# Performance work log

Measured on AMD Instinct MI355X. Metric: run time of the kernel, lower is better.

Reference implementation:

```python
import jax, jax.numpy as jnp
import numpy as np

N, F, H, Z = 80, 64, 256, 128
OFF = N * (N - 1) // 2  # 3160
E = 800
MPM_ITERS = 50


def _gcn(x, src, dst, W, b, n):
    # PyG GCNConv: add self-loops, symmetric normalization D^-1/2 (A+I) D^-1/2, then +bias
    h = x @ W
    ones = jnp.ones(src.shape[0], dtype=h.dtype)
    deg = jax.ops.segment_sum(ones, dst, num_segments=n)
    dinv = jax.lax.rsqrt(jnp.maximum(deg, 1e-12))
    norm = dinv[src] * dinv[dst]
    out = jax.ops.segment_sum(h[src] * norm[:, None], dst, num_segments=n)
    return out + b


def _bn(h, g, b):
    # BatchNorm1d, training mode (biased batch stats), eps=1e-5
    m = h.mean(0)
    v = ((h - m) ** 2).mean(0)
    return g * (h - m) * jax.lax.rsqrt(v + 1e-5) + b


def setup_inputs() -> dict:
    key = jax.random.key(0)
    ks = jax.random.split(key, 32)
    rn = lambda k, s, sc=0.05: (jax.random.normal(k, s, dtype=jnp.float32) * sc)
    inp = {
        'x': jax.random.normal(ks[0], (N, F), dtype=jnp.float32),
        'edge_index': jax.random.randint(ks[1], (2, E), 0, N, dtype=jnp.int32),
        'adj': jax.random.randint(ks[2], (N, N), 0, 2, dtype=jnp.int32),
        'eps': jax.random.normal(ks[3], (1, Z), dtype=jnp.float32),
        'W1': rn(ks[4], (F, H)), 'b1': jnp.zeros((H,), jnp.float32),
        'g1': jnp.ones((H,), jnp.float32), 'bt1': jnp.zeros((H,), jnp.float32),
        'W2': rn(ks[5], (H, H)), 'b2': jnp.zeros((H,), jnp.float32),
        'g2': jnp.ones((H,), jnp.float32), 'bt2': jnp.zeros((H,), jnp.float32),
        'Wmu': rn(ks[6], (H, Z)), 'bmu': jnp.zeros((Z,), jnp.float32),
        'Wlv': rn(ks[7], (H, Z)), 'blv': jnp.zeros((Z,), jnp.float32),
        'We1': rn(ks[8], (Z, H)), 'be1': jnp.zeros((H,), jnp.float32),
        'We2': rn(ks[9], (H, OFF)), 'be2': jnp.zeros((OFF,), jnp.float32),
        'Wn1': rn(ks[10], (Z, H)), 'bn1': jnp.zeros((H,), jnp.float32),
        'Wn2': rn(ks[11], (H, N)), 'bn2': jnp.zeros((N,), jnp.float32),
    }
    return inp


def reference(x, edge_index, adj, eps, W1, b1, g1, bt1, W2, b2, g2, bt2,
              Wmu, bmu, Wlv, blv, We1, be1, We2, be2, Wn1, bn1, Wn2, bn2):
    n = N
    # ---- encoder: GCN -> BN -> ReLU (x2), mean pool over real nodes ----
    sl = jnp.arange(n, dtype=edge_index.dtype)
    src = jnp.concatenate([edge_index[0], sl])
    dst = jnp.concatenate([edge_index[1], sl])
    h = jax.nn.relu(_bn(_gcn(x, src, dst, W1, b1, n), g1, bt1))
    h = jax.nn.relu(_bn(_gcn(h, src, dst, W2, b2, n), g2, bt2))
    g_vec = h.sum(0, keepdims=True) / n  # [1,H], R_int == n
    mu = g_vec @ Wmu + bmu
    logvar = jnp.clip(g_vec @ Wlv + blv, -4.0, 4.0)
    z = mu + eps * jnp.exp(0.5 * logvar)  # reparam
    # ---- decoder ----
    vec_logits = (jax.nn.relu(z @ We1 + be1) @ We2 + be2)[0]   # [OFF]
    node_logits = (jax.nn.relu(z @ Wn1 + bn1) @ Wn2 + bn2)[0]  # [N]
    iu, ju = np.triu_indices(n, k=1)
    A_hat = jnp.zeros((n, n), jnp.float32).at[iu, ju].set(vec_logits)
    A_hat = A_hat + A_hat.T
    d = jnp.arange(n)
    A_hat = A_hat.at[d, d].set(node_logits)  # A_hat_logits
    # ---- edge similarity tensor S [N,N,N,N] ----
    A = jnp.maximum(adj, adj.T).astype(jnp.float32)
    A = A.at[d, d].set(1.0)
    B = jax.nn.sigmoid(A_hat).at[d, d].set(1.0)
    degA, degB = A.sum(1), B.sum(1)
    node_sim = 1.0 / (jnp.abs(degA[:, None] - degB[None, :]) + 1.0)
    dA, dB = jnp.diag(A), jnp.diag(B)  # all ones by construction (faithful to source)
    S = (A * dA[:, None] * dA[None, :])[:, :, None, None] * \
        (B * dB[:, None] * dB[None, :])[None, None, :, :]
    eye = jnp.eye(n, dtype=bool)
    xor = eye[:, :, None, None] ^ eye[None, None, :, :]
    S = jnp.where(xor, 0.0, S)
    both = eye[:, :, None, None] & eye[None, None, :, :]
    S = jnp.where(both, node_sim[:, None, :, None], S)
    # ---- MPM fixed point (fixed 50 iterations) ----
    notey = (~eye).astype(S.dtype)[:, :, None]  # [i,j,1]
    X0 = jnp.full((n, n), 1.0 / n, dtype=jnp.float32)

    def step(X, _):
        node_term = X * node_sim
        XS_max = jnp.max(S * X[None, :, None, :], axis=-1)  # [i,j,a] = max_b X[j,b]*S[i,j,a,b]
        edge_term = jnp.sum(XS_max * notey, axis=1)          # sum over j != i
        Xn = node_term + edge_term
        Xn = Xn / jnp.linalg.norm(Xn)
        return Xn, None

    X, _ = jax.lax.scan(step, X0, None, length=MPM_ITERS)
    return X
```

## Files before the change

### kernel.cpp

```cpp
#include <hip/hip_runtime.h>


#define NN 80
#define PBLK 20
#define TPB 320
#define RP 84
#define NCOLS 13

__device__ __forceinline__ void gbar(int* ctr, int target){
  __syncthreads();
  if (threadIdx.x == 0){
    __hip_atomic_fetch_add(ctr, 1, __ATOMIC_RELEASE, __HIP_MEMORY_SCOPE_AGENT);
    while (__hip_atomic_load(ctr, __ATOMIC_ACQUIRE, __HIP_MEMORY_SCOPE_AGENT) < target)
      __builtin_amdgcn_s_sleep(1);
  }
  __syncthreads();
}

__device__ __forceinline__ float wave_sum(float v){
  #pragma unroll
  for (int k = 32; k >= 1; k >>= 1) v += __shfl_xor(v, k, 64);
  return v;
}

__device__ void gcn_bn_relu(const float* inL, float* outT,
                            const float* bias, const float* gamma, const float* beta,
                            const int* ei, const float* dinv,
                            float* accL, float* colstat, int p, int tid)
{
  for (int u = tid; u < NCOLS*NN; u += TPB) accL[u] = 0.f;
  __syncthreads();
  for (int cl = 0; cl < NCOLS; cl++){
    int c = p + PBLK*cl; if (c >= 256) break;
    const float* col = &inL[cl*NN];
    for (int e = tid; e < 800; e += TPB){
      int sidx = ei[e], didx = ei[800+e];
      atomicAdd(&accL[cl*NN + didx], col[sidx]*dinv[sidx]*dinv[didx]);
    }
  }
  __syncthreads();
  for (int u = tid; u < NCOLS*NN; u += TPB){
    int cl = u/NN, i = u - cl*NN, c = p + PBLK*cl;
    if (c < 256) accL[u] += inL[cl*NN+i]*dinv[i]*dinv[i] + bias[c];
  }
  __syncthreads();
  if (tid < NCOLS){
    int c = p + PBLK*tid;
    if (c < 256){
      const float* a = &accL[tid*NN];
      float m = 0.f;
      for (int i = 0; i < NN; i++) m += a[i];
      m *= (1.0f/NN);
      float v = 0.f;
      for (int i = 0; i < NN; i++){ float d = a[i]-m; v += d*d; }
      v *= (1.0f/NN);
      colstat[2*tid]   = m;
      colstat[2*tid+1] = 1.0f/sqrtf(v + 1e-5f);
    }
  }
  __syncthreads();
  for (int u = tid; u < NCOLS*NN; u += TPB){
    int cl = u/NN, i = u - cl*NN, c = p + PBLK*cl;
    if (c < 256){
      float hv = gamma[c]*(accL[u]-colstat[2*cl])*colstat[2*cl+1] + beta[c];
      outT[c*NN+i] = fmaxf(hv, 0.f);
    }
  }
}

__global__ __launch_bounds__(TPB, 1) void gvae_fused(
    const float* __restrict__ x,  const int* __restrict__ ei, const int* __restrict__ adj,
    const float* __restrict__ eps,
    const float* __restrict__ W1, const float* __restrict__ b1, const float* __restrict__ g1, const float* __restrict__ bt1,
    const float* __restrict__ W2, const float* __restrict__ b2, const float* __restrict__ g2, const float* __restrict__ bt2,
    const float* __restrict__ Wmu,const float* __restrict__ bmu,const float* __restrict__ Wlv,const float* __restrict__ blv,
    const float* __restrict__ We1,const float* __restrict__ be1,const float* __restrict__ We2,const float* __restrict__ be2,
    float* __restrict__ out, float* __restrict__ ws)
{
  const int tid = threadIdx.x;
  const int p   = blockIdx.x;

  int*   ctr   = (int*)ws;
  float* sumsq = ws + 16;
  float* hT    = ws + 128;
  float* h2T   = hT  + 20480;
  float* Bm    = h2T + 20480;
  float* Xb0   = Bm  + 6400;
  float* Xb1   = Xb0 + 6400;

  __shared__ float Xs[NN*RP];
  __shared__ float MtL[4*RP];
  __shared__ float red[8];
  __shared__ float dinv[NN];
  __shared__ float accL[NCOLS*NN];
  __shared__ float hL[NCOLS*NN];
  __shared__ float gv[256], zv[128], t1v[256];
  __shared__ float colstat[2*NCOLS];

  for (int i = tid; i < NN; i += TPB) accL[i] = 1.0f;
  __syncthreads();
  for (int e = tid; e < 800; e += TPB) atomicAdd(&accL[ei[800+e]], 1.0f);
  __syncthreads();
  for (int i = tid; i < NN; i += TPB) dinv[i] = 1.0f/sqrtf(accL[i]);
  __syncthreads();

  for (int u = tid; u < NCOLS*NN; u += TPB){
    int cl = u/NN, i = u - cl*NN, c = p + PBLK*cl;
    if (c < 256){
      float s = 0.f;
      for (int k = 0; k < 64; k++) s += x[i*64+k]*W1[k*256+c];
      hL[u] = s;
    }
  }
  __syncthreads();
  gcn_bn_relu(hL, hT, b1, g1, bt1, ei, dinv, accL, colstat, p, tid);
  gbar(ctr, 1*PBLK);

  for (int u = tid; u < 20*NCOLS; u += TPB){
    int cl = u/20, iq = u - cl*20, c = p + PBLK*cl;
    if (c < 256){
      int i0 = 4*iq;
      float a0=0.f,a1=0.f,a2=0.f,a3=0.f;
      for (int k = 0; k < 256; k++){
        float wv = W2[k*256+c];
        float4 hv = *(const float4*)&hT[k*NN+i0];
        a0 += hv.x*wv; a1 += hv.y*wv; a2 += hv.z*wv; a3 += hv.w*wv;
      }
      hL[cl*NN+i0+0]=a0; hL[cl*NN+i0+1]=a1; hL[cl*NN+i0+2]=a2; hL[cl*NN+i0+3]=a3;
    }
  }
  __syncthreads();
  gcn_bn_relu(hL, h2T, b2, g2, bt2, ei, dinv, accL, colstat, p, tid);
  gbar(ctr, 2*PBLK);

  for (int c = tid; c < 256; c += TPB){
    const float* r = &h2T[c*NN];
    float s = 0.f;
    for (int i = 0; i < NN; i++) s += r[i];
    gv[c] = s*(1.0f/NN);
  }
  __syncthreads();
  for (int c = tid; c < 128; c += TPB){
    float smu = bmu[c], slv = blv[c];
    for (int k = 0; k < 256; k++){
      float g = gv[k];
      smu += g*Wmu[k*128+c];
      slv += g*Wlv[k*128+c];
    }
    slv = fminf(fmaxf(slv, -4.f), 4.f);
    zv[c] = smu + eps[c]*expf(0.5f*slv);
  }
  __syncthreads();
  for (int c = tid; c < 256; c += TPB){
    float s = be1[c];
    for (int k = 0; k < 128; k++) s += zv[k]*We1[k*256+c];
    t1v[c] = fmaxf(s, 0.f);
  }
  __syncthreads();
  for (int r = 0; r < 4; r++){
    int i = p + PBLK*r;
    if (tid == 0) Bm[i*NN+i] = 1.0f;
    for (int j = i+1+tid; j < NN; j += TPB){
      int off = i*(2*NN-1-i)/2 + (j-i-1);
      float s = be2[off];
      for (int k = 0; k < 256; k++) s += t1v[k]*We2[k*3160+off];
      float sg = 1.0f/(1.0f + expf(-s));
      Bm[i*NN+j] = sg;
      Bm[j*NN+i] = sg;
    }
  }
  gbar(ctr, 3*PBLK);

  const int w  = tid >> 6;
  const int l  = tid & 63;
  const int il = 16*w + (l & 15);
  const int ae = l >> 4;
  const int al = 4*p + ae;

  float4 Af[20], Bf[20];
  float degA = 0.f, degB = 0.f;
  #pragma unroll
  for (int c = 0; c < 20; c++){
    int j0 = 4*c;
    int4 ar = *(const int4*)&adj[il*NN+j0];
    int q0 = adj[(j0+0)*NN+il];
    int q1 = adj[(j0+1)*NN+il];
    int q2 = adj[(j0+2)*NN+il];
    int q3 = adj[(j0+3)*NN+il];
    float4 a;
    a.x = ((ar.x|q0) != 0 || il == j0+0) ? 1.f : 0.f;
    a.y = ((ar.y|q1) != 0 || il == j0+1) ? 1.f : 0.f;
    a.z = ((ar.z|q2) != 0 || il == j0+2) ? 1.f : 0.f;
    a.w = ((ar.w|q3) != 0 || il == j0+3) ? 1.f : 0.f;
    Af[c] = a;
    degA += (a.x+a.y)+(a.z+a.w);
  }
  #pragma unroll
  for (int c = 0; c < 20; c++){
    float4 b = *(const float4*)&Bm[al*NN+4*c];
    Bf[c] = b;
    degB += (b.x+b.y)+(b.z+b.w);
  }
  const float ns = 1.0f/(fabsf(degA-degB)+1.0f);
  #pragma unroll
  for (int c = 0; c < 20; c++){
    if (c == p){
      if      (ae == 0) Bf[c].x = 0.f;
      else if (ae == 1) Bf[c].y = 0.f;
      else if (ae == 2) Bf[c].z = 0.f;
      else              Bf[c].w = 0.f;
    }
  }

  for (int u = tid; u < NN*RP; u += TPB) Xs[u] = 1.0f/NN;
  float xn = 0.f;
  int bar = 3;
  for (int t = 0; t < 50; t++){
    if (t > 0){
      const float* Xsrc = ((t-1)&1) ? Xb1 : Xb0;
      for (int u = tid; u < NN*20; u += TPB){
        int j = u/20, c4 = (u - j*20)*4;
        *(float4*)&Xs[j*RP+c4] = *(const float4*)&Xsrc[j*NN+c4];
      }
    }
    __syncthreads();
    float sc = 1.0f;
    if (t > 0)
      sc = 1.0f/sqrtf(__hip_atomic_load(&sumsq[t], __ATOMIC_RELAXED, __HIP_MEMORY_SCOPE_AGENT));

    float m = 0.f;
    #pragma unroll
    for (int c = 0; c < 20; c++){
      float4 xv = *(const float4*)&Xs[il*RP+4*c];
      float p0 = xv.x*Bf[c].x, p1 = xv.y*Bf[c].y, p2 = xv.z*Bf[c].z, p3 = xv.w*Bf[c].w;
      m = fmaxf(m, fmaxf(fmaxf(p0,p1), fmaxf(p2,p3)));
    }
    float xnode = Xs[il*RP+al];
    MtL[ae*RP+il] = m;
    __syncthreads();

    float e0=0.f,e1=0.f,e2=0.f,e3=0.f;
    #pragma unroll
    for (int c = 0; c < 20; c++){
      float4 mv = *(const float4*)&MtL[ae*RP+4*c];
      e0 += Af[c].x*mv.x; e1 += Af[c].y*mv.y; e2 += Af[c].z*mv.z; e3 += Af[c].w*mv.w;
    }
    float edge = ((e0+e1)+(e2+e3)) - m;
    xn = sc*(ns*xnode + edge);

    if (t < 49){
      float* Xdst = (t&1) ? Xb1 : Xb0;
      Xdst[il*NN+al] = xn;
    }
    float v = wave_sum(xn*xn);
    if (l == 0) red[w] = v;
    __syncthreads();
    if (tid == 0){
      float tot = ((red[0]+red[1])+(red[2]+red[3]))+red[4];
      __hip_atomic_fetch_add(&sumsq[t+1], tot, __ATOMIC_RELAXED, __HIP_MEMORY_SCOPE_AGENT);
    }
    bar++;
    gbar(ctr, bar*PBLK);
  }
  float sf = 1.0f/sqrtf(__hip_atomic_load(&sumsq[50], __ATOMIC_RELAXED, __HIP_MEMORY_SCOPE_AGENT));
  out[il*NN+al] = xn*sf;
}

extern "C" void kernel_launch(void* const* d_in, const int* in_sizes, int n_in,
                              void* d_out, int out_size, void* d_ws, size_t ws_size,
                              hipStream_t stream)
{
  (void)in_sizes; (void)n_in; (void)out_size; (void)ws_size;
  hipMemsetAsync(d_ws, 0, 512, stream);
  gvae_fused<<<PBLK, TPB, 0, stream>>>(
      (const float*)d_in[0],  (const int*)d_in[1],   (const int*)d_in[2],   (const float*)d_in[3],
      (const float*)d_in[4],  (const float*)d_in[5],  (const float*)d_in[6],  (const float*)d_in[7],
      (const float*)d_in[8],  (const float*)d_in[9],  (const float*)d_in[10], (const float*)d_in[11],
      (const float*)d_in[12], (const float*)d_in[13], (const float*)d_in[14], (const float*)d_in[15],
      (const float*)d_in[16], (const float*)d_in[17], (const float*)d_in[18], (const float*)d_in[19],
      (float*)d_out, (float*)d_ws);
}
```

Before: 510.8 us.

## Replace global counter barriers with per-block flags and per-iteration norm slots

Removes the atomic-counter grid barrier and replaces it with per-block flag stores that every block polls, plus per-iteration partial-sum slots that consumers poll until they are nonzero. This merges the barrier with the norm reduction in the 50-iteration MPM loop. Global-memory traffic now uses relaxed agent-scope atomic loads and stores. It also parallelises the BN statistics with shuffles, computes the graph-mean pooling locally instead of writing h2T, and moves the adjacency loads ahead of the barrier wait. The risks are memory-ordering issues from relaxed loads and stores without acquire/release fences, and a hang if any partial sum is exactly zero.

```diff
diff --git a/kernel.cpp b/kernel.cpp
--- a/kernel.cpp
+++ b/kernel.cpp
@@ -7,14 +7,26 @@
 #define RP 84
 #define NCOLS 13
 
-__device__ __forceinline__ void gbar(int* ctr, int target){
-  __syncthreads();
-  if (threadIdx.x == 0){
-    __hip_atomic_fetch_add(ctr, 1, __ATOMIC_RELEASE, __HIP_MEMORY_SCOPE_AGENT);
-    while (__hip_atomic_load(ctr, __ATOMIC_ACQUIRE, __HIP_MEMORY_SCOPE_AGENT) < target)
-      __builtin_amdgcn_s_sleep(1);
-  }
-  __syncthreads();
+__device__ __forceinline__ float ld_f32g(const float* p){
+  return __hip_atomic_load((float*)p, __ATOMIC_RELAXED, __HIP_MEMORY_SCOPE_AGENT);
+}
+__device__ __forceinline__ void st_f32g(float* p, float v){
+  __hip_atomic_store(p, v, __ATOMIC_RELAXED, __HIP_MEMORY_SCOPE_AGENT);
+}
+__device__ __forceinline__ int ld_i32g(const int* p){
+  return __hip_atomic_load((int*)p, __ATOMIC_RELAXED, __HIP_MEMORY_SCOPE_AGENT);
+}
+__device__ __forceinline__ void st_i32g(int* p, int v){
+  __hip_atomic_store(p, v, __ATOMIC_RELAXED, __HIP_MEMORY_SCOPE_AGENT);
+}
+__device__ __forceinline__ float2 ld_f2g(const float* p){
+  union { unsigned long long u; float2 f; } c;
+  c.u = __hip_atomic_load((unsigned long long*)p, __ATOMIC_RELAXED, __HIP_MEMORY_SCOPE_AGENT);
+  return c.f;
+}
+__device__ __forceinline__ void st_f2g(float* p, float a, float b){
+  union { unsigned long long u; float2 f; } c; c.f.x = a; c.f.y = b;
+  __hip_atomic_store((unsigned long long*)p, c.u, __ATOMIC_RELAXED, __HIP_MEMORY_SCOPE_AGENT);
 }
 
 __device__ __forceinline__ float wave_sum(float v){
@@ -23,9 +35,8 @@
   return v;
 }
 
-__device__ void gcn_bn_relu(const float* inL, float* outT,
-                            const float* bias, const float* gamma, const float* beta,
-                            const int* ei, const float* dinv,
+__device__ void gcn_bn_relu(const float* inL, const float* bias, const float* gamma,
+                            const float* beta, const int* ei, const float* dinvS,
                             float* accL, float* colstat, int p, int tid)
 {
   for (int u = tid; u < NCOLS*NN; u += TPB) accL[u] = 0.f;
@@ -34,38 +45,46 @@
     int c = p + PBLK*cl; if (c >= 256) break;
     const float* col = &inL[cl*NN];
     for (int e = tid; e < 800; e += TPB){
-      int sidx = ei[e], didx = ei[800+e];
-      atomicAdd(&accL[cl*NN + didx], col[sidx]*dinv[sidx]*dinv[didx]);
+      int s = ei[e], d = ei[800+e];
+      atomicAdd(&accL[cl*NN + d], col[s]*dinvS[s]*dinvS[d]);
     }
   }
   __syncthreads();
   for (int u = tid; u < NCOLS*NN; u += TPB){
     int cl = u/NN, i = u - cl*NN, c = p + PBLK*cl;
-    if (c < 256) accL[u] += inL[cl*NN+i]*dinv[i]*dinv[i] + bias[c];
-  }
-  __syncthreads();
-  if (tid < NCOLS){
-    int c = p + PBLK*tid;
-    if (c < 256){
-      const float* a = &accL[tid*NN];
-      float m = 0.f;
-      for (int i = 0; i < NN; i++) m += a[i];
-      m *= (1.0f/NN);
-      float v = 0.f;
-      for (int i = 0; i < NN; i++){ float d = a[i]-m; v += d*d; }
-      v *= (1.0f/NN);
-      colstat[2*tid]   = m;
-      colstat[2*tid+1] = 1.0f/sqrtf(v + 1e-5f);
+    if (c < 256) accL[u] += inL[u]*dinvS[i]*dinvS[i] + bias[c];
+  }
+  __syncthreads();
+  if (tid < 16*NCOLS){
+    int g = tid >> 4, s = tid & 15, c = p + PBLK*g;
+    if (c < 256){
+      float r[5];
+      float sm = 0.f;
+      #pragma unroll
+      for (int i = 0; i < 5; i++){ r[i] = accL[g*NN + s + 16*i]; sm += r[i]; }
+      #pragma unroll
+      for (int k = 1; k < 16; k <<= 1) sm += __shfl_xor(sm, k, 64);
+      float m = sm*(1.0f/NN);
+      float sq = 0.f;
+      #pragma unroll
+      for (int i = 0; i < 5; i++){ float d = r[i]-m; sq += d*d; }
+      #pragma unroll
+      for (int k = 1; k < 16; k <<= 1) sq += __shfl_xor(sq, k, 64);
+      if (s == 0){
+        colstat[2*g]   = m;
+        colstat[2*g+1] = 1.0f/sqrtf(sq*(1.0f/NN) + 1e-5f);
+      }
     }
   }
   __syncthreads();
   for (int u = tid; u < NCOLS*NN; u += TPB){
-    int cl = u/NN, i = u - cl*NN, c = p + PBLK*cl;
+    int cl = u/NN, c = p + PBLK*cl;
     if (c < 256){
       float hv = gamma[c]*(accL[u]-colstat[2*cl])*colstat[2*cl+1] + beta[c];
-      outT[c*NN+i] = fmaxf(hv, 0.f);
-    }
-  }
+      accL[u] = fmaxf(hv, 0.f);
+    }
+  }
+  __syncthreads();
 }
 
 __global__ __launch_bounds__(TPB, 1) void gvae_fused(
@@ -80,18 +99,19 @@
   const int tid = threadIdx.x;
   const int p   = blockIdx.x;
 
-  int*   ctr   = (int*)ws;
-  float* sumsq = ws + 16;
-  float* hT    = ws + 128;
-  float* h2T   = hT  + 20480;
-  float* Bm    = h2T + 20480;
-  float* Xb0   = Bm  + 6400;
+  int*   flag  = (int*)ws;
+  float* slots = ws + 32;
+  float* gvS   = ws + 1056;
+  float* hT    = ws + 1312;
+  float* Bm    = hT + 20480;
+  float* Xb0   = Bm + 6400;
   float* Xb1   = Xb0 + 6400;
 
   __shared__ float Xs[NN*RP];
   __shared__ float MtL[4*RP];
   __shared__ float red[8];
-  __shared__ float dinv[NN];
+  __shared__ float scS;
+  __shared__ float dinvS[NN];
   __shared__ float accL[NCOLS*NN];
   __shared__ float hL[NCOLS*NN];
   __shared__ float gv[256], zv[128], t1v[256];
@@ -101,7 +121,7 @@
   __syncthreads();
   for (int e = tid; e < 800; e += TPB) atomicAdd(&accL[ei[800+e]], 1.0f);
   __syncthreads();
-  for (int i = tid; i < NN; i += TPB) dinv[i] = 1.0f/sqrtf(accL[i]);
+  for (int i = tid; i < NN; i += TPB) dinvS[i] = 1.0f/sqrtf(accL[i]);
   __syncthreads();
 
   for (int u = tid; u < NCOLS*NN; u += TPB){
@@ -113,9 +133,16 @@
     }
   }
   __syncthreads();
-  gcn_bn_relu(hL, hT, b1, g1, bt1, ei, dinv, accL, colstat, p, tid);
-  gbar(ctr, 1*PBLK);
-
+  gcn_bn_relu(hL, b1, g1, bt1, ei, dinvS, accL, colstat, p, tid);
+  for (int u2 = tid; u2 < 40*NCOLS; u2 += TPB){
+    int cl = u2/40, i2 = (u2 - cl*40)*2, c = p + PBLK*cl;
+    if (c < 256) st_f2g(&hT[c*NN+i2], accL[cl*NN+i2], accL[cl*NN+i2+1]);
+  }
+  __syncthreads();
+  if (tid == 0) st_i32g(&flag[p], 1);
+
+  if (tid < PBLK) while (ld_i32g(&flag[tid]) < 1) {}
+  __syncthreads();
   for (int u = tid; u < 20*NCOLS; u += TPB){
     int cl = u/20, iq = u - cl*20, c = p + PBLK*cl;
     if (c < 256){
@@ -123,24 +150,35 @@
       float a0=0.f,a1=0.f,a2=0.f,a3=0.f;
       for (int k = 0; k < 256; k++){
         float wv = W2[k*256+c];
-        float4 hv = *(const float4*)&hT[k*NN+i0];
-        a0 += hv.x*wv; a1 += hv.y*wv; a2 += hv.z*wv; a3 += hv.w*wv;
+        float2 h01 = ld_f2g(&hT[k*NN+i0]);
+        float2 h23 = ld_f2g(&hT[k*NN+i0+2]);
+        a0 += h01.x*wv; a1 += h01.y*wv; a2 += h23.x*wv; a3 += h23.y*wv;
       }
       hL[cl*NN+i0+0]=a0; hL[cl*NN+i0+1]=a1; hL[cl*NN+i0+2]=a2; hL[cl*NN+i0+3]=a3;
     }
   }
   __syncthreads();
-  gcn_bn_relu(hL, h2T, b2, g2, bt2, ei, dinv, accL, colstat, p, tid);
-  gbar(ctr, 2*PBLK);
-
-  for (int c = tid; c < 256; c += TPB){
-    const float* r = &h2T[c*NN];
-    float s = 0.f;
-    for (int i = 0; i < NN; i++) s += r[i];
-    gv[c] = s*(1.0f/NN);
-  }
-  __syncthreads();
-  for (int c = tid; c < 128; c += TPB){
+  gcn_bn_relu(hL, b2, g2, bt2, ei, dinvS, accL, colstat, p, tid);
+  if (tid < 16*NCOLS){
+    int g = tid >> 4, s = tid & 15, c = p + PBLK*g;
+    if (c < 256){
+      float sm = 0.f;
+      #pragma unroll
+      for (int i = 0; i < 5; i++) sm += accL[g*NN + s + 16*i];
+      #pragma unroll
+      for (int k = 1; k < 16; k <<= 1) sm += __shfl_xor(sm, k, 64);
+      if (s == 0) st_f32g(&gvS[c], sm*(1.0f/NN));
+    }
+  }
+  __syncthreads();
+  if (tid == 0) st_i32g(&flag[p], 2);
+
+  if (tid < PBLK) while (ld_i32g(&flag[tid]) < 2) {}
+  __syncthreads();
+  if (tid < 256) gv[tid] = ld_f32g(&gvS[tid]);
+  __syncthreads();
+  if (tid < 128){
+    int c = tid;
     float smu = bmu[c], slv = blv[c];
     for (int k = 0; k < 256; k++){
       float g = gv[k];
@@ -151,25 +189,36 @@
     zv[c] = smu + eps[c]*expf(0.5f*slv);
   }
   __syncthreads();
-  for (int c = tid; c < 256; c += TPB){
-    float s = be1[c];
-    for (int k = 0; k < 128; k++) s += zv[k]*We1[k*256+c];
-    t1v[c] = fmaxf(s, 0.f);
-  }
-  __syncthreads();
-  for (int r = 0; r < 4; r++){
-    int i = p + PBLK*r;
-    if (tid == 0) Bm[i*NN+i] = 1.0f;
-    for (int j = i+1+tid; j < NN; j += TPB){
-      int off = i*(2*NN-1-i)/2 + (j-i-1);
+  if (tid < 256){
+    float s = be1[tid];
+    for (int k = 0; k < 128; k++) s += zv[k]*We1[k*256+tid];
+    t1v[tid] = fmaxf(s, 0.f);
+  }
+  __syncthreads();
+
+  {
+    int c0 = 79-p, c1 = 59-p, c2 = 39-p, c3 = 19-p;
+    int t1b = c0+c1, t2b = t1b+c2, L = t2b+c3;
+    int i = -1, j = -1;
+    if      (tid < c0) { i = p;    j = p+1 +tid;        }
+    else if (tid < t1b){ i = p+20; j = p+21+(tid-c0);   }
+    else if (tid < t2b){ i = p+40; j = p+41+(tid-t1b);  }
+    else if (tid < L)  { i = p+60; j = p+61+(tid-t2b);  }
+    if (i >= 0){
+      int off = i*(159-i)/2 + (j-i-1);
       float s = be2[off];
       for (int k = 0; k < 256; k++) s += t1v[k]*We2[k*3160+off];
       float sg = 1.0f/(1.0f + expf(-s));
-      Bm[i*NN+j] = sg;
-      Bm[j*NN+i] = sg;
-    }
-  }
-  gbar(ctr, 3*PBLK);
+      st_f32g(&Bm[i*NN+j], sg);
+      st_f32g(&Bm[j*NN+i], sg);
+    }
+    if (tid >= 316){
+      int r = tid-316, ii = p+20*r;
+      st_f32g(&Bm[ii*NN+ii], 1.0f);
+    }
+  }
+  __syncthreads();
+  if (tid == 0) st_i32g(&flag[p], 3);
 
   const int w  = tid >> 6;
   const int l  = tid & 63;
@@ -177,8 +226,8 @@
   const int ae = l >> 4;
   const int al = 4*p + ae;
 
-  float4 Af[20], Bf[20];
-  float degA = 0.f, degB = 0.f;
+  float4 Af[20];
+  float degA = 0.f;
   #pragma unroll
   for (int c = 0; c < 20; c++){
     int j0 = 4*c;
@@ -195,38 +244,57 @@
     Af[c] = a;
     degA += (a.x+a.y)+(a.z+a.w);
   }
+
+  if (tid < PBLK) while (ld_i32g(&flag[tid]) < 3) {}
+  __syncthreads();
+
+  float4 Bf[20];
+  float degB = 0.f;
   #pragma unroll
   for (int c = 0; c < 20; c++){
-    float4 b = *(const float4*)&Bm[al*NN+4*c];
-    Bf[c] = b;
-    degB += (b.x+b.y)+(b.z+b.w);
+    float2 b01 = ld_f2g(&Bm[al*NN+4*c]);
+    float2 b23 = ld_f2g(&Bm[al*NN+4*c+2]);
+    Bf[c].x = b01.x; Bf[c].y = b01.y; Bf[c].z = b23.x; Bf[c].w = b23.y;
+    degB += (b01.x+b01.y)+(b23.x+b23.y);
   }
   const float ns = 1.0f/(fabsf(degA-degB)+1.0f);
-  #pragma unroll
-  for (int c = 0; c < 20; c++){
-    if (c == p){
-      if      (ae == 0) Bf[c].x = 0.f;
-      else if (ae == 1) Bf[c].y = 0.f;
-      else if (ae == 2) Bf[c].z = 0.f;
-      else              Bf[c].w = 0.f;
-    }
+  {
+    if      (ae == 0) Bf[p].x = 0.f;
+    else if (ae == 1) Bf[p].y = 0.f;
+    else if (ae == 2) Bf[p].z = 0.f;
+    else              Bf[p].w = 0.f;
   }
 
   for (int u = tid; u < NN*RP; u += TPB) Xs[u] = 1.0f/NN;
+  __syncthreads();
   float xn = 0.f;
-  int bar = 3;
   for (int t = 0; t < 50; t++){
+    float sc = 1.0f;
     if (t > 0){
+      float pv = 0.f;
+      if (tid < PBLK){
+        const float* sp = &slots[(t-1)*PBLK + tid];
+        do { pv = ld_f32g(sp); } while (pv == 0.0f);
+      }
+      if (w == 0){
+        float v = pv;
+        #pragma unroll
+        for (int k = 1; k < 32; k <<= 1) v += __shfl_xor(v, k, 64);
+        if (tid == 0) scS = 1.0f/sqrtf(v);
+      }
+      __syncthreads();
+      sc = scS;
       const float* Xsrc = ((t-1)&1) ? Xb1 : Xb0;
-      for (int u = tid; u < NN*20; u += TPB){
-        int j = u/20, c4 = (u - j*20)*4;
-        *(float4*)&Xs[j*RP+c4] = *(const float4*)&Xsrc[j*NN+c4];
-      }
-    }
-    __syncthreads();
-    float sc = 1.0f;
-    if (t > 0)
-      sc = 1.0f/sqrtf(__hip_atomic_load(&sumsq[t], __ATOMIC_RELAXED, __HIP_MEMORY_SCOPE_AGENT));
+      #pragma unroll
+      for (int q = 0; q < 10; q++){
+        int p2 = tid + TPB*q;
+        int j = p2/40, c2 = p2 - 40*j;
+        float2 xv = ld_f2g(&Xsrc[j*NN + 2*c2]);
+        Xs[j*RP + 2*c2]     = xv.x;
+        Xs[j*RP + 2*c2 + 1] = xv.y;
+      }
+      __syncthreads();
+    }
 
     float m = 0.f;
     #pragma unroll
@@ -250,20 +318,32 @@
 
     if (t < 49){
       float* Xdst = (t&1) ? Xb1 : Xb0;
-      Xdst[il*NN+al] = xn;
-    }
-    float v = wave_sum(xn*xn);
-    if (l == 0) red[w] = v;
+      st_f32g(&Xdst[il*NN+al], xn);
+    }
+    float v2 = wave_sum(xn*xn);
+    if (l == 0) red[w] = v2;
     __syncthreads();
     if (tid == 0){
       float tot = ((red[0]+red[1])+(red[2]+red[3]))+red[4];
-      __hip_atomic_fetch_add(&sumsq[t+1], tot, __ATOMIC_RELAXED, __HIP_MEMORY_SCOPE_AGENT);
-    }
-    bar++;
-    gbar(ctr, bar*PBLK);
-  }
-  float sf = 1.0f/sqrtf(__hip_atomic_load(&sumsq[50], __ATOMIC_RELAXED, __HIP_MEMORY_SCOPE_AGENT));
-  out[il*NN+al] = xn*sf;
+      st_f32g(&slots[t*PBLK+p], tot);
+    }
+  }
+
+  {
+    float pv = 0.f;
+    if (tid < PBLK){
+      const float* sp = &slots[49*PBLK + tid];
+      do { pv = ld_f32g(sp); } while (pv == 0.0f);
+    }
+    if (w == 0){
+      float v = pv;
+      #pragma unroll
+      for (int k = 1; k < 32; k <<= 1) v += __shfl_xor(v, k, 64);
+      if (tid == 0) scS = 1.0f/sqrtf(v);
+    }
+    __syncthreads();
+    out[il*NN+al] = xn * scS;
+  }
 }
 
 extern "C" void kernel_launch(void* const* d_in, const int* in_sizes, int n_in,
@@ -271,7 +351,7 @@
                               hipStream_t stream)
 {
   (void)in_sizes; (void)n_in; (void)out_size; (void)ws_size;
-  hipMemsetAsync(d_ws, 0, 512, stream);
+  hipMemsetAsync(d_ws, 0, 4224, stream);
   gvae_fused<<<PBLK, TPB, 0, stream>>>(
       (const float*)d_in[0],  (const int*)d_in[1],   (const int*)d_in[2],   (const float*)d_in[3],
       (const float*)d_in[4],  (const float*)d_in[5],  (const float*)d_in[6],  (const float*)d_in[7],
```

Result: slower. 568.9 us (+11.4%).
